# Kernel optimization log

Hardware: AMD Instinct MI355X
Metric: run time of the kernel (lower is better)

## Reference

```python
import jax, jax.numpy as jnp
import numpy as np

NUM_USERS = 100000
NUM_ITEMS = 50000
NUM_BRANDS = 1000
N_NODES = NUM_USERS + NUM_ITEMS + NUM_BRANDS
EMBED_DIM = 64
N_LAYERS = 3
N_EDGES = 10000000


def setup_inputs() -> dict:
    key = jax.random.key(0)
    k1, k2, k3, k4, k5, k6 = jax.random.split(key, 6)
    adj_rows = jax.random.randint(k1, (N_EDGES,), 0, N_NODES, dtype=jnp.int64 if jax.config.jax_enable_x64 else jnp.int32)
    adj_cols = jax.random.randint(k2, (N_EDGES,), 0, N_NODES, dtype=jnp.int64 if jax.config.jax_enable_x64 else jnp.int32)
    adj_vals = jax.random.uniform(k3, (N_EDGES,), dtype=jnp.float32)
    user_emb = jax.random.normal(k4, (NUM_USERS, EMBED_DIM), dtype=jnp.float32)
    item_emb = jax.random.normal(k5, (NUM_ITEMS, EMBED_DIM), dtype=jnp.float32)
    brand_emb = jax.random.normal(k6, (NUM_BRANDS, EMBED_DIM), dtype=jnp.float32)
    return {
        "adj_rows": adj_rows,
        "adj_cols": adj_cols,
        "adj_vals": adj_vals,
        "user_emb": user_emb,
        "item_emb": item_emb,
        "brand_emb": brand_emb,
    }


def _spmm(rows, cols, vals, x, n_nodes):
    # y = A @ x for sparse COO A: gather source rows, scale, scatter-add to dest rows
    return jax.ops.segment_sum(vals[:, None] * x[cols], rows, num_segments=n_nodes)


def reference(adj_rows, adj_cols, adj_vals, user_emb, item_emb, brand_emb):
    n_users = user_emb.shape[0]
    n_items = item_emb.shape[0]
    n_nodes = n_users + n_items + brand_emb.shape[0]
    ego = jnp.concatenate([user_emb, item_emb, brand_emb], axis=0)  # [N, D]
    acc = ego  # running sum over layers (fused stack+mean)
    for _ in range(N_LAYERS):
        ego = _spmm(adj_rows, adj_cols, adj_vals, ego, n_nodes)
        acc = acc + ego
    final = acc / jnp.asarray(N_LAYERS + 1, dtype=acc.dtype)
    final_user = final[:n_users]
    final_item = final[n_users:n_users + n_items]
    final_brand = final[n_users + n_items:]
    return (final_user, final_item, final_brand, user_emb, item_emb)
```

## Files before the change

### kernel.cpp

```cpp
#include <hip/hip_runtime.h>
#include <hip/hip_bf16.h>
#include <stdint.h>

#define NU 100000
#define NI 50000
#define NB 1000
#define NN 151000
#define D  64
#define NE 10000000

#define BSH   6
#define BROWS 64
#define NBUCK 2360
#define CAPB  5632
#define BINB  512
#define BINT  1024

typedef unsigned short u16;
typedef unsigned int   u32;

__device__ __forceinline__ u16 f2bf(float f) {
    union { float f; u32 i; } c; c.f = f;
    u32 lsb = (c.i >> 16) & 1;
    c.i += 0x7fffu + lsb;
    return (u16)(c.i >> 16);
}

__global__ __launch_bounds__(BINT) void k_bin(
    const int* __restrict__ rows, const int* __restrict__ cols,
    const float* __restrict__ vals,
    int* __restrict__ bucketcur, int2* __restrict__ subbuf) {
    __shared__ int hcnt[NBUCK];
    __shared__ int hcur[NBUCK];
    int b = blockIdx.x, tid = threadIdx.x;
    long e0 = (long)b * NE / BINB;
    long e1 = (long)(b + 1) * NE / BINB;
    for (int j = tid; j < NBUCK; j += BINT) hcnt[j] = 0;
    __syncthreads();
    for (long i = e0 + tid; i < e1; i += BINT)
        atomicAdd(&hcnt[rows[i] >> BSH], 1);
    __syncthreads();
    for (int j = tid; j < NBUCK; j += BINT) {
        int c = hcnt[j];
        hcur[j] = c ? atomicAdd(&bucketcur[j], c) : 0;
    }
    __syncthreads();
    for (long i = e0 + tid; i < e1; i += BINT) {
        int r  = rows[i];
        int bk = r >> BSH;
        int pos = atomicAdd(&hcur[bk], 1);
        if (pos < CAPB)
            subbuf[(size_t)bk * CAPB + pos] =
                make_int2(((r & (BROWS - 1)) << 18) | cols[i], __float_as_int(vals[i]));
    }
}

__global__ __launch_bounds__(256) void k_csr(
    const int* __restrict__ bucketcur, const int2* __restrict__ subbuf,
    int* __restrict__ off, int* __restrict__ cnt, int* __restrict__ gtotal,
    int2* __restrict__ cicv) {
    __shared__ int rcnt[BROWS], rexc[BROWS], lcur[BROWS];
    __shared__ int sbase;
    __shared__ int2 sbuf[CAPB];
    int b = blockIdx.x, tid = threadIdx.x;
    int T = bucketcur[b]; if (T > CAPB) T = CAPB;
    if (tid < BROWS) rcnt[tid] = 0;
    __syncthreads();
    const int2* src = subbuf + (size_t)b * CAPB;
    for (int j = tid; j < T; j += 256)
        atomicAdd(&rcnt[(u32)src[j].x >> 18], 1);
    __syncthreads();
    if (tid < 64) {
        int v = rcnt[tid], x = v;
        for (int d = 1; d < 64; d <<= 1) {
            int t = __shfl_up(x, d);
            if (tid >= d) x += t;
        }
        rexc[tid] = x - v;
        if (tid == 63) sbase = atomicAdd(gtotal, x);
    }
    __syncthreads();
    int base = sbase;
    if (tid < BROWS) {
        int r = b * BROWS + tid;
        if (r < NN) { off[r] = base + rexc[tid]; cnt[r] = rcnt[tid]; }
        lcur[tid] = rexc[tid];
    }
    __syncthreads();
    for (int j = tid; j < T; j += 256) {
        int2 rec = src[j];
        int rl = (u32)rec.x >> 18;
        int dst = atomicAdd(&lcur[rl], 1);
        sbuf[dst] = make_int2(rec.x & 0x3FFFF, rec.y);
    }
    __syncthreads();
    for (int j = tid; j < T; j += 256)
        cicv[base + j] = sbuf[j];
}

__global__ void k_init(const float4* __restrict__ ue, const float4* __restrict__ ie,
                       const float4* __restrict__ be, ushort4* __restrict__ xa,
                       float4* __restrict__ acc) {
    int i4 = blockIdx.x * blockDim.x + threadIdx.x;
    if (i4 >= NN * D / 4) return;
    float4 v;
    if (i4 < NU * D / 4)             v = ue[i4];
    else if (i4 < (NU + NI) * D / 4) v = ie[i4 - NU * D / 4];
    else                             v = be[i4 - (NU + NI) * D / 4];
    acc[i4] = v;
    ushort4 h;
    h.x = f2bf(v.x); h.y = f2bf(v.y); h.z = f2bf(v.z); h.w = f2bf(v.w);
    xa[i4] = h;
}

__device__ __forceinline__ void acc8(float f, uint4 h, float* s) {
    union { u32 i; float v; } t;
    t.i = h.x << 16;         s[0] += f * t.v;
    t.i = h.x & 0xffff0000u; s[1] += f * t.v;
    t.i = h.y << 16;         s[2] += f * t.v;
    t.i = h.y & 0xffff0000u; s[3] += f * t.v;
    t.i = h.z << 16;         s[4] += f * t.v;
    t.i = h.z & 0xffff0000u; s[5] += f * t.v;
    t.i = h.w << 16;         s[6] += f * t.v;
    t.i = h.w & 0xffff0000u; s[7] += f * t.v;
}

template<int LAST>
__global__ __launch_bounds__(256) void k_spmm(
    const int* __restrict__ off, const int* __restrict__ cnt,
    const int2* __restrict__ cicv,
    const u16* __restrict__ xin, uint4* __restrict__ xout,
    float4* __restrict__ acc, float4* __restrict__ out) {
    int gid  = blockIdx.x * blockDim.x + threadIdx.x;
    int row  = gid >> 6;
    int lane = threadIdx.x & 63;
    if (row >= NN) return;
    int base = __builtin_amdgcn_readfirstlane(off[row]);
    int deg  = __builtin_amdgcn_readfirstlane(cnt[row]);
    int q = lane >> 3;
    int p = lane & 7;
    float s[8] = {0.f, 0.f, 0.f, 0.f, 0.f, 0.f, 0.f, 0.f};
    for (int e = 0; e < deg; e += 32) {
        int2 r0 = cicv[base + e + q];
        int2 r1 = cicv[base + e + 8 + q];
        int2 r2 = cicv[base + e + 16 + q];
        int2 r3 = cicv[base + e + 24 + q];
        bool ok0 = (e + q)      < deg;
        bool ok1 = (e + 8 + q)  < deg;
        bool ok2 = (e + 16 + q) < deg;
        bool ok3 = (e + 24 + q) < deg;
        int c0 = ok0 ? r0.x : 0;  float f0 = ok0 ? __int_as_float(r0.y) : 0.f;
        int c1 = ok1 ? r1.x : 0;  float f1 = ok1 ? __int_as_float(r1.y) : 0.f;
        int c2 = ok2 ? r2.x : 0;  float f2 = ok2 ? __int_as_float(r2.y) : 0.f;
        int c3 = ok3 ? r3.x : 0;  float f3 = ok3 ? __int_as_float(r3.y) : 0.f;
        uint4 h0 = *(const uint4*)(xin + (size_t)c0 * D + p * 8);
        uint4 h1 = *(const uint4*)(xin + (size_t)c1 * D + p * 8);
        uint4 h2 = *(const uint4*)(xin + (size_t)c2 * D + p * 8);
        uint4 h3 = *(const uint4*)(xin + (size_t)c3 * D + p * 8);
        acc8(f0, h0, s);
        acc8(f1, h1, s);
        acc8(f2, h2, s);
        acc8(f3, h3, s);
    }
#pragma unroll
    for (int k = 0; k < 8; ++k) {
        s[k] += __shfl_xor(s[k], 8);
        s[k] += __shfl_xor(s[k], 16);
        s[k] += __shfl_xor(s[k], 32);
    }
    int o16 = row * 16 + p * 2;
    if (LAST) {
        if (q == 0) {
            float4 a0 = acc[o16], a1 = acc[o16 + 1];
            out[o16]     = make_float4((a0.x + s[0]) * 0.25f, (a0.y + s[1]) * 0.25f,
                                       (a0.z + s[2]) * 0.25f, (a0.w + s[3]) * 0.25f);
            out[o16 + 1] = make_float4((a1.x + s[4]) * 0.25f, (a1.y + s[5]) * 0.25f,
                                       (a1.z + s[6]) * 0.25f, (a1.w + s[7]) * 0.25f);
        }
    } else {
        if (q == 0) {
            float4 a0 = acc[o16], a1 = acc[o16 + 1];
            acc[o16]     = make_float4(a0.x + s[0], a0.y + s[1], a0.z + s[2], a0.w + s[3]);
            acc[o16 + 1] = make_float4(a1.x + s[4], a1.y + s[5], a1.z + s[6], a1.w + s[7]);
        } else if (q == 1) {
            uint4 hh;
            hh.x = (u32)f2bf(s[0]) | ((u32)f2bf(s[1]) << 16);
            hh.y = (u32)f2bf(s[2]) | ((u32)f2bf(s[3]) << 16);
            hh.z = (u32)f2bf(s[4]) | ((u32)f2bf(s[5]) << 16);
            hh.w = (u32)f2bf(s[6]) | ((u32)f2bf(s[7]) << 16);
            xout[row * 8 + p] = hh;
        }
    }
}

extern "C" void kernel_launch(void* const* d_in, const int* in_sizes, int n_in,
                              void* d_out, int out_size, void* d_ws, size_t ws_size,
                              hipStream_t stream) {
    const int*   rows = (const int*)d_in[0];
    const int*   cols = (const int*)d_in[1];
    const float* vals = (const float*)d_in[2];
    float* out = (float*)d_out;

    char* w = (char*)d_ws;
    size_t p = 0;
#define WALLOC(var, type, count) \
    type* var = (type*)(w + p); p += (((size_t)(count) * sizeof(type)) + 255) & ~(size_t)255;
    WALLOC(bucketcur, int, NBUCK)
    WALLOC(gtotal,    int, 64)
    WALLOC(off,       int, NN)
    WALLOC(cnt,       int, NN)
    size_t regA = p;
    int2* subbuf = (int2*)(w + regA);
    size_t subbuf_sz = ((size_t)NBUCK * CAPB * sizeof(int2) + 255) & ~(size_t)255;
    u16*   xa  = (u16*)(w + regA);
    u16*   xb  = (u16*)(w + regA + (size_t)NN * D * sizeof(u16));
    float* acc = (float*)(w + regA + 2 * (size_t)NN * D * sizeof(u16));
    p = regA + subbuf_sz;
    WALLOC(cicv, int2, (size_t)NE + 32)
#undef WALLOC
    (void)p; (void)ws_size; (void)in_sizes; (void)n_in; (void)out_size;

    hipMemsetAsync(bucketcur, 0, (size_t)NBUCK * sizeof(int), stream);
    hipMemsetAsync(gtotal, 0, sizeof(int), stream);

    k_bin<<<BINB, BINT, 0, stream>>>(rows, cols, vals, bucketcur, subbuf);
    k_csr<<<NBUCK, 256, 0, stream>>>(bucketcur, subbuf, off, cnt, gtotal, cicv);
    k_init<<<(NN * D / 4 + 255) / 256, 256, 0, stream>>>(
        (const float4*)d_in[3], (const float4*)d_in[4],
        (const float4*)d_in[5], (ushort4*)xa, (float4*)acc);

    int spmm_blocks = NN / 4;
    k_spmm<0><<<spmm_blocks, 256, 0, stream>>>(off, cnt, cicv, xa, (uint4*)xb,
                                               (float4*)acc, (float4*)out);
    k_spmm<0><<<spmm_blocks, 256, 0, stream>>>(off, cnt, cicv, xb, (uint4*)xa,
                                               (float4*)acc, (float4*)out);
    k_spmm<1><<<spmm_blocks, 256, 0, stream>>>(off, cnt, cicv, xa, (uint4*)xb,
                                               (float4*)acc, (float4*)out);

    hipMemcpyAsync(out + (size_t)NN * D, d_in[3], (size_t)NU * D * sizeof(float),
                   hipMemcpyDeviceToDevice, stream);
    hipMemcpyAsync(out + (size_t)NN * D + (size_t)NU * D, d_in[4],
                   (size_t)NI * D * sizeof(float), hipMemcpyDeviceToDevice, stream);
}
```

Measured before the change: 989.6 us.

## Replace global bucket atomics with per-block prefix binning; fuse output copy into init

The binning kernel now computes a block-local exclusive scan of its bucket histogram and writes records into its own contiguous slice of the edge range. The per-block offsets go to a prefix array, which replaces the global atomic bucket cursors and the fixed per-bucket capacity slabs. The CSR kernel then gathers each bucket's pieces from all 512 bin blocks, with each thread walking a short segment serially, so its reads are less coalesced. Separately, the user and item passthrough outputs are written inside the init kernel instead of by two device-to-device memcpys, which saves a re-read of those embeddings.

```diff
diff --git a/kernel.cpp b/kernel.cpp
--- a/kernel.cpp
+++ b/kernel.cpp
@@ -15,6 +15,7 @@
 #define CAPB  5632
 #define BINB  512
 #define BINT  1024
+#define PSTR  2368
 
 typedef unsigned short u16;
 typedef unsigned int   u32;
@@ -29,9 +30,10 @@
 __global__ __launch_bounds__(BINT) void k_bin(
     const int* __restrict__ rows, const int* __restrict__ cols,
     const float* __restrict__ vals,
-    int* __restrict__ bucketcur, int2* __restrict__ subbuf) {
+    int* __restrict__ prefarr, int2* __restrict__ subbuf) {
     __shared__ int hcnt[NBUCK];
     __shared__ int hcur[NBUCK];
+    __shared__ int tsum[BINT];
     int b = blockIdx.x, tid = threadIdx.x;
     long e0 = (long)b * NE / BINB;
     long e1 = (long)(b + 1) * NE / BINB;
@@ -40,35 +42,59 @@
     for (long i = e0 + tid; i < e1; i += BINT)
         atomicAdd(&hcnt[rows[i] >> BSH], 1);
     __syncthreads();
-    for (int j = tid; j < NBUCK; j += BINT) {
-        int c = hcnt[j];
-        hcur[j] = c ? atomicAdd(&bucketcur[j], c) : 0;
-    }
+    int base3 = tid * 3;
+    int v0 = (base3     < NBUCK) ? hcnt[base3]     : 0;
+    int v1 = (base3 + 1 < NBUCK) ? hcnt[base3 + 1] : 0;
+    int v2 = (base3 + 2 < NBUCK) ? hcnt[base3 + 2] : 0;
+    int lsum = v0 + v1 + v2;
+    tsum[tid] = lsum;
+    __syncthreads();
+    for (int d = 1; d < BINT; d <<= 1) {
+        int t = (tid >= d) ? tsum[tid - d] : 0;
+        __syncthreads();
+        tsum[tid] += t;
+        __syncthreads();
+    }
+    int excl = tsum[tid] - lsum;
+    int* prow = prefarr + (size_t)b * PSTR;
+    if (base3     < NBUCK) { hcur[base3]     = excl;           prow[base3]     = excl; }
+    if (base3 + 1 < NBUCK) { hcur[base3 + 1] = excl + v0;      prow[base3 + 1] = excl + v0; }
+    if (base3 + 2 < NBUCK) { hcur[base3 + 2] = excl + v0 + v1; prow[base3 + 2] = excl + v0 + v1; }
+    if (tid == BINT - 1) prow[NBUCK] = tsum[tid];
     __syncthreads();
     for (long i = e0 + tid; i < e1; i += BINT) {
         int r  = rows[i];
         int bk = r >> BSH;
         int pos = atomicAdd(&hcur[bk], 1);
-        if (pos < CAPB)
-            subbuf[(size_t)bk * CAPB + pos] =
-                make_int2(((r & (BROWS - 1)) << 18) | cols[i], __float_as_int(vals[i]));
+        subbuf[e0 + pos] =
+            make_int2(((r & (BROWS - 1)) << 18) | cols[i], __float_as_int(vals[i]));
     }
 }
 
 __global__ __launch_bounds__(256) void k_csr(
-    const int* __restrict__ bucketcur, const int2* __restrict__ subbuf,
+    const int* __restrict__ prefarr, const int2* __restrict__ subbuf,
     int* __restrict__ off, int* __restrict__ cnt, int* __restrict__ gtotal,
     int2* __restrict__ cicv) {
     __shared__ int rcnt[BROWS], rexc[BROWS], lcur[BROWS];
-    __shared__ int sbase;
+    __shared__ int csta[BINB], clen[BINB];
+    __shared__ int sbase, stot;
     __shared__ int2 sbuf[CAPB];
     int b = blockIdx.x, tid = threadIdx.x;
-    int T = bucketcur[b]; if (T > CAPB) T = CAPB;
+    for (int blk = tid; blk < BINB; blk += 256) {
+        const int* prow = prefarr + (size_t)blk * PSTR;
+        int s = prow[b];
+        int e = prow[b + 1];
+        csta[blk] = (int)((long)blk * NE / BINB) + s;
+        clen[blk] = e - s;
+    }
     if (tid < BROWS) rcnt[tid] = 0;
     __syncthreads();
-    const int2* src = subbuf + (size_t)b * CAPB;
-    for (int j = tid; j < T; j += 256)
-        atomicAdd(&rcnt[(u32)src[j].x >> 18], 1);
+    for (int blk = tid; blk < BINB; blk += 256) {
+        const int2* src = subbuf + csta[blk];
+        int l = clen[blk];
+        for (int k = 0; k < l; ++k)
+            atomicAdd(&rcnt[(u32)src[k].x >> 18], 1);
+    }
     __syncthreads();
     if (tid < 64) {
         int v = rcnt[tid], x = v;
@@ -77,7 +103,10 @@
             if (tid >= d) x += t;
         }
         rexc[tid] = x - v;
-        if (tid == 63) sbase = atomicAdd(gtotal, x);
+        if (tid == 63) {
+            stot = x;
+            sbase = atomicAdd(gtotal, x);
+        }
     }
     __syncthreads();
     int base = sbase;
@@ -87,20 +116,25 @@
         lcur[tid] = rexc[tid];
     }
     __syncthreads();
-    for (int j = tid; j < T; j += 256) {
-        int2 rec = src[j];
-        int rl = (u32)rec.x >> 18;
-        int dst = atomicAdd(&lcur[rl], 1);
-        sbuf[dst] = make_int2(rec.x & 0x3FFFF, rec.y);
-    }
-    __syncthreads();
+    for (int blk = tid; blk < BINB; blk += 256) {
+        const int2* src = subbuf + csta[blk];
+        int l = clen[blk];
+        for (int k = 0; k < l; ++k) {
+            int2 rec = src[k];
+            int rl = (u32)rec.x >> 18;
+            int dst = atomicAdd(&lcur[rl], 1);
+            if (dst < CAPB) sbuf[dst] = make_int2(rec.x & 0x3FFFF, rec.y);
+        }
+    }
+    __syncthreads();
+    int T = stot; if (T > CAPB) T = CAPB;
     for (int j = tid; j < T; j += 256)
         cicv[base + j] = sbuf[j];
 }
 
 __global__ void k_init(const float4* __restrict__ ue, const float4* __restrict__ ie,
                        const float4* __restrict__ be, ushort4* __restrict__ xa,
-                       float4* __restrict__ acc) {
+                       float4* __restrict__ acc, float4* __restrict__ out4) {
     int i4 = blockIdx.x * blockDim.x + threadIdx.x;
     if (i4 >= NN * D / 4) return;
     float4 v;
@@ -111,6 +145,8 @@
     ushort4 h;
     h.x = f2bf(v.x); h.y = f2bf(v.y); h.z = f2bf(v.z); h.w = f2bf(v.w);
     xa[i4] = h;
+    if (i4 < (NU + NI) * D / 4)
+        out4[NN * D / 4 + i4] = v;
 }
 
 __device__ __forceinline__ void acc8(float f, uint4 h, float* s) {
@@ -205,13 +241,13 @@
     size_t p = 0;
 #define WALLOC(var, type, count) \
     type* var = (type*)(w + p); p += (((size_t)(count) * sizeof(type)) + 255) & ~(size_t)255;
-    WALLOC(bucketcur, int, NBUCK)
-    WALLOC(gtotal,    int, 64)
-    WALLOC(off,       int, NN)
-    WALLOC(cnt,       int, NN)
+    WALLOC(gtotal,  int, 64)
+    WALLOC(off,     int, NN)
+    WALLOC(cnt,     int, NN)
+    WALLOC(prefarr, int, (size_t)BINB * PSTR)
     size_t regA = p;
     int2* subbuf = (int2*)(w + regA);
-    size_t subbuf_sz = ((size_t)NBUCK * CAPB * sizeof(int2) + 255) & ~(size_t)255;
+    size_t subbuf_sz = ((size_t)NE * sizeof(int2) + 255) & ~(size_t)255;
     u16*   xa  = (u16*)(w + regA);
     u16*   xb  = (u16*)(w + regA + (size_t)NN * D * sizeof(u16));
     float* acc = (float*)(w + regA + 2 * (size_t)NN * D * sizeof(u16));
@@ -220,14 +256,13 @@
 #undef WALLOC
     (void)p; (void)ws_size; (void)in_sizes; (void)n_in; (void)out_size;
 
-    hipMemsetAsync(bucketcur, 0, (size_t)NBUCK * sizeof(int), stream);
     hipMemsetAsync(gtotal, 0, sizeof(int), stream);
 
-    k_bin<<<BINB, BINT, 0, stream>>>(rows, cols, vals, bucketcur, subbuf);
-    k_csr<<<NBUCK, 256, 0, stream>>>(bucketcur, subbuf, off, cnt, gtotal, cicv);
+    k_bin<<<BINB, BINT, 0, stream>>>(rows, cols, vals, prefarr, subbuf);
+    k_csr<<<NBUCK, 256, 0, stream>>>(prefarr, subbuf, off, cnt, gtotal, cicv);
     k_init<<<(NN * D / 4 + 255) / 256, 256, 0, stream>>>(
         (const float4*)d_in[3], (const float4*)d_in[4],
-        (const float4*)d_in[5], (ushort4*)xa, (float4*)acc);
+        (const float4*)d_in[5], (ushort4*)xa, (float4*)acc, (float4*)out);
 
     int spmm_blocks = NN / 4;
     k_spmm<0><<<spmm_blocks, 256, 0, stream>>>(off, cnt, cicv, xa, (uint4*)xb,
@@ -236,9 +271,4 @@
                                                (float4*)acc, (float4*)out);
     k_spmm<1><<<spmm_blocks, 256, 0, stream>>>(off, cnt, cicv, xa, (uint4*)xb,
                                                (float4*)acc, (float4*)out);
-
-    hipMemcpyAsync(out + (size_t)NN * D, d_in[3], (size_t)NU * D * sizeof(float),
-                   hipMemcpyDeviceToDevice, stream);
-    hipMemcpyAsync(out + (size_t)NN * D + (size_t)NU * D, d_in[4],
-                   (size_t)NI * D * sizeof(float), hipMemcpyDeviceToDevice, stream);
-}
+}
```

Result: slower. 1.034 ms (+4.5%).
